# Kernel tuning notes

Hardware: AMD Instinct MI355X
Metric: run time of the kernel (lower is better)

The kernel has to match this reference:

```python
import jax, jax.numpy as jnp
import numpy as np

N, E, G, H, C = 50000, 800000, 512, 4, 64
DIN, DENC = 128, 256


def setup_inputs() -> dict:
    key = jax.random.key(0)
    ks = jax.random.split(key, 12)
    inp = {
        "hy": jax.random.normal(ks[0], (1, G, DENC), jnp.float32),
        "x": jax.random.normal(ks[1], (N, DIN), jnp.float32),
        "edge_index": jax.random.randint(ks[2], (2, E), 0, N, jnp.int32),
        "batch": jnp.sort(jax.random.randint(ks[3], (N,), 0, G, jnp.int32)),
        # GATv2Conv params (lin_l, lin_r: DIN -> H*C; att: [H, C]; bias: [C] since concat=False)
        "Wl": jax.random.normal(ks[4], (DIN, H * C), jnp.float32) * (1.0 / np.sqrt(DIN)),
        "bl": jnp.zeros((H * C,), jnp.float32),
        "Wr": jax.random.normal(ks[5], (DIN, H * C), jnp.float32) * (1.0 / np.sqrt(DIN)),
        "br": jnp.zeros((H * C,), jnp.float32),
        "att": jax.random.normal(ks[6], (H, C), jnp.float32) * (1.0 / np.sqrt(C)),
        "bias_gnn": jnp.zeros((C,), jnp.float32),
        # fc: (DENC + 64) -> DENC
        "Wfc": jax.random.normal(ks[7], (DENC + C, DENC), jnp.float32) * (1.0 / np.sqrt(DENC + C)),
        "bfc": jnp.zeros((DENC,), jnp.float32),
    }
    return inp


def _gatv2(x, edge_index, Wl, bl, Wr, br, att, bias_gnn):
    # add self loops (PyG default)
    loops = jnp.arange(N, dtype=edge_index.dtype)
    src = jnp.concatenate([edge_index[0], loops])
    dst = jnp.concatenate([edge_index[1], loops])
    xl = (x @ Wl + bl).reshape(N, H, C)  # source transform
    xr = (x @ Wr + br).reshape(N, H, C)  # target transform
    s = jax.nn.leaky_relu(xl[src] + xr[dst], 0.2)        # [Et, H, C]
    e = jnp.einsum('ehc,hc->eh', s, att)                 # [Et, H]
    # segment softmax over incoming edges of each dst node
    m = jax.ops.segment_max(e, dst, num_segments=N)
    m = jnp.where(jnp.isfinite(m), m, 0.0)
    a = jnp.exp(e - m[dst])
    denom = jax.ops.segment_sum(a, dst, num_segments=N)
    alpha = a / (denom[dst] + 1e-16)                     # [Et, H]
    msg = xl[src] * alpha[:, :, None]                    # [Et, H, C]
    out = jax.ops.segment_sum(msg, dst, num_segments=N)  # [N, H, C]
    return out.mean(axis=1) + bias_gnn                   # concat=False -> head mean


def reference(hy, x, edge_index, batch, Wl, bl, Wr, br, att, bias_gnn, Wfc, bfc):
    h = jax.nn.leaky_relu(_gatv2(x, edge_index, Wl, bl, Wr, br, att, bias_gnn), 0.01)
    # global mean pool per graph
    sums = jax.ops.segment_sum(h, batch, num_segments=G)
    cnts = jax.ops.segment_sum(jnp.ones((N, 1), h.dtype), batch, num_segments=G)
    hg = (sums / jnp.maximum(cnts, 1.0))[None]           # [1, G, C]
    cat = jnp.concatenate([hy, hg], axis=2)              # [1, G, DENC+C]
    return cat @ Wfc + bfc
```

## Files before the change

### kernel.cpp

```cpp
#include <hip/hip_runtime.h>

typedef unsigned short u16;
typedef __attribute__((ext_vector_type(8))) short bf16x8;
typedef __attribute__((ext_vector_type(4))) float f32x4;
typedef __attribute__((ext_vector_type(2))) float f32x2;

constexpr int N    = 50000;
constexpr int E    = 800000;
constexpr int G    = 512;
constexpr int HC   = 256;
constexpr int DIN  = 128;
constexpr int DENC = 256;
constexpr int DFC  = 320;
constexpr int NBLK = (N + 1023) / 1024;
constexpr int MT   = 64;
constexpr int XB   = (N + MT - 1) / MT;
constexpr int CBLK = 4;

__device__ __forceinline__ float bf2f(u16 u) {
    return __uint_as_float(((unsigned)u) << 16);
}
__device__ __forceinline__ u16 f2bf(float f) {
    unsigned u = __float_as_uint(f);
    u += 0x7fffu + ((u >> 16) & 1u);
    return (u16)(u >> 16);
}
__device__ __forceinline__ float lrelu(float v, float s) {
    return v > 0.0f ? v : v * s;
}

template<int CTRL>
__device__ __forceinline__ float dpp_radd(float x) {
    int y = __builtin_amdgcn_update_dpp(0, __float_as_int(x), CTRL, 0xF, 0xF, true);
    return x + __int_as_float(y);
}

template<bool BF> __device__ __forceinline__ float ld(const void* p, size_t i) {
    if constexpr (BF) return bf2f(((const u16*)p)[i]);
    else              return ((const float*)p)[i];
}
template<bool BF> __device__ __forceinline__ float4 ld4(const void* p, size_t i) {
    if constexpr (BF) {
        ushort4 v = ((const ushort4*)p)[i >> 2];
        return make_float4(bf2f(v.x), bf2f(v.y), bf2f(v.z), bf2f(v.w));
    } else {
        return ((const float4*)p)[i >> 2];
    }
}
template<bool BF> __device__ __forceinline__ void st(void* p, size_t i, float v) {
    if constexpr (BF) ((u16*)p)[i] = f2bf(v);
    else              ((float*)p)[i] = v;
}
__device__ __forceinline__ float ldr(const void* p, size_t i, bool bf) {
    return bf ? bf2f(((const u16*)p)[i]) : ((const float*)p)[i];
}

__global__ void k_detect(const void* x, int* flag) {
    if (blockIdx.x == 0 && threadIdx.x == 0) {
        const u16* p = (const u16*)x;
        int ok = 0;
        for (int i = 0; i < 256; i++) {
            unsigned e = (p[i] >> 7) & 0xffu;
            if (e == 0u || (e >= 100u && e <= 140u)) ok++;
        }
        *flag = (ok >= 218) ? 0 : 1;
    }
}

__global__ __launch_bounds__(64) void k_wprep(const void* Wl, const void* Wr,
                                              u16* __restrict__ whi, u16* __restrict__ wlo,
                                              const int* __restrict__ flag) {
    bool bf = (*flag == 0);
    int tile = blockIdx.x;
    int l = threadIdx.x;
    int c = tile & 31, s = tile >> 5;
    int col = c * 16 + (l & 15);
    int kbase = s * 32 + ((l >> 4) * 8);
    size_t o = (size_t)tile * 512 + (size_t)l * 8;
    #pragma unroll
    for (int j = 0; j < 8; j++) {
        int k = kbase + j;
        float v = (col < HC) ? ldr(Wl, (size_t)k * HC + col, bf)
                             : ldr(Wr, (size_t)k * HC + (col - HC), bf);
        u16 h = f2bf(v);
        whi[o + j] = h;
        wlo[o + j] = f2bf(v - bf2f(h));
    }
}

template<bool BF>
__global__ __launch_bounds__(256, 4) void k_xlxr_t(
    const void* __restrict__ x, const u16* __restrict__ whi, const u16* __restrict__ wlo,
    const void* __restrict__ bl, const void* __restrict__ br,
    u16* __restrict__ xl, u16* __restrict__ xr, const int* __restrict__ flag) {
    if ((*flag == 0) != BF) return;
    __shared__ u16 ah[(BF ? 1 : 2) * MT][136];
    int b = blockIdx.x, t = threadIdx.x;
    int rb = b >> 1, cg = b & 1;
    int row0 = rb * MT;

    {
        int k0 = (t & 15) * 8;
        #pragma unroll
        for (int it = 0; it < 4; it++) {
            int r = (t >> 4) + it * 16;
            int g = row0 + r; if (g >= N) g = N - 1;
            size_t base = (size_t)g * DIN + k0;
            if constexpr (BF) {
                const ushort4* xp = (const ushort4*)x;
                *(ushort4*)&ah[r][k0]     = xp[base >> 2];
                *(ushort4*)&ah[r][k0 + 4] = xp[(base >> 2) + 1];
            } else {
                const float4* xp = (const float4*)x;
                float4 f0 = xp[base >> 2], f1 = xp[(base >> 2) + 1];
                float v[8] = {f0.x, f0.y, f0.z, f0.w, f1.x, f1.y, f1.z, f1.w};
                #pragma unroll
                for (int j = 0; j < 8; j++) {
                    u16 h = f2bf(v[j]);
                    ah[r][k0 + j] = h;
                    ah[MT + r][k0 + j] = f2bf(v[j] - bf2f(h));
                }
            }
        }
    }
    __syncthreads();

    int w = t >> 6, l = t & 63;
    int rl = l & 15, kg = (l >> 4) * 8;
    f32x4 acc[4][CBLK];
    #pragma unroll
    for (int rt = 0; rt < 4; rt++)
        #pragma unroll
        for (int ci = 0; ci < CBLK; ci++) {
            f32x4 z = {0.f, 0.f, 0.f, 0.f};
            acc[rt][ci] = z;
        }

    #pragma unroll
    for (int s = 0; s < 4; s++) {
        bf16x8 a0 = *(const bf16x8*)&ah[rl][s * 32 + kg];
        bf16x8 a1 = *(const bf16x8*)&ah[16 + rl][s * 32 + kg];
        bf16x8 a2 = *(const bf16x8*)&ah[32 + rl][s * 32 + kg];
        bf16x8 a3 = *(const bf16x8*)&ah[48 + rl][s * 32 + kg];
        #pragma unroll
        for (int ci = 0; ci < CBLK; ci++) {
            int c = cg * 16 + w * CBLK + ci;
            size_t fo = ((size_t)(s * 32 + c) * 64 + l) * 8;
            bf16x8 bh = *(const bf16x8*)&whi[fo];
            acc[0][ci] = __builtin_amdgcn_mfma_f32_16x16x32_bf16(a0, bh, acc[0][ci], 0, 0, 0);
            acc[1][ci] = __builtin_amdgcn_mfma_f32_16x16x32_bf16(a1, bh, acc[1][ci], 0, 0, 0);
            acc[2][ci] = __builtin_amdgcn_mfma_f32_16x16x32_bf16(a2, bh, acc[2][ci], 0, 0, 0);
            acc[3][ci] = __builtin_amdgcn_mfma_f32_16x16x32_bf16(a3, bh, acc[3][ci], 0, 0, 0);
            if constexpr (!BF) {
                bf16x8 e0 = *(const bf16x8*)&ah[MT + rl][s * 32 + kg];
                bf16x8 e1 = *(const bf16x8*)&ah[MT + 16 + rl][s * 32 + kg];
                bf16x8 e2 = *(const bf16x8*)&ah[MT + 32 + rl][s * 32 + kg];
                bf16x8 e3 = *(const bf16x8*)&ah[MT + 48 + rl][s * 32 + kg];
                bf16x8 bw = *(const bf16x8*)&wlo[fo];
                acc[0][ci] = __builtin_amdgcn_mfma_f32_16x16x32_bf16(a0, bw, acc[0][ci], 0, 0, 0);
                acc[0][ci] = __builtin_amdgcn_mfma_f32_16x16x32_bf16(e0, bh, acc[0][ci], 0, 0, 0);
                acc[1][ci] = __builtin_amdgcn_mfma_f32_16x16x32_bf16(a1, bw, acc[1][ci], 0, 0, 0);
                acc[1][ci] = __builtin_amdgcn_mfma_f32_16x16x32_bf16(e1, bh, acc[1][ci], 0, 0, 0);
                acc[2][ci] = __builtin_amdgcn_mfma_f32_16x16x32_bf16(a2, bw, acc[2][ci], 0, 0, 0);
                acc[2][ci] = __builtin_amdgcn_mfma_f32_16x16x32_bf16(e2, bh, acc[2][ci], 0, 0, 0);
                acc[3][ci] = __builtin_amdgcn_mfma_f32_16x16x32_bf16(a3, bw, acc[3][ci], 0, 0, 0);
                acc[3][ci] = __builtin_amdgcn_mfma_f32_16x16x32_bf16(e3, bh, acc[3][ci], 0, 0, 0);
            }
        }
    }
    __syncthreads();

    float fbias[CBLK];
    #pragma unroll
    for (int ci = 0; ci < CBLK; ci++) {
        int colm = ((cg * 16 + w * CBLK + ci) * 16 + (l & 15)) & (HC - 1);
        fbias[ci] = ld<BF>(cg ? br : bl, colm);
    }
    u16* dst = cg ? xr : xl;

    u16 (*ep)[264] = reinterpret_cast<u16 (*)[264]>(&ah[0][0]);
    int r4 = (l >> 4) * 4;
    #pragma unroll
    for (int rt = 0; rt < 4; rt++) {
        #pragma unroll
        for (int ci = 0; ci < CBLK; ci++) {
            int colm = ((cg * 16 + w * CBLK + ci) * 16 + (l & 15)) & (HC - 1);
            #pragma unroll
            for (int i = 0; i < 4; i++)
                ep[r4 + i][colm] = f2bf(acc[rt][ci][i] + fbias[ci]);
        }
        __syncthreads();
        #pragma unroll
        for (int j = 0; j < 2; j++) {
            int q   = t + 256 * j;
            int row = q >> 5;
            int ck  = q & 31;
            int gr  = row0 + rt * 16 + row;
            uint4 v = *(const uint4*)&ep[row][ck * 8];
            if (gr < N) *(uint4*)&dst[(size_t)gr * HC + ck * 8] = v;
        }
        __syncthreads();
    }
}

__global__ void k_deg(const int* __restrict__ ei, int* __restrict__ deg) {
    int e = blockIdx.x * blockDim.x + threadIdx.x;
    if (e < E) {
        int d = ei[E + e];
        if ((unsigned)d < (unsigned)N) atomicAdd(&deg[d], 1);
    }
}

__global__ void k_chunksum(const int* __restrict__ deg, int* __restrict__ blocksum) {
    int b = blockIdx.x, t = threadIdx.x;
    int base = b * 1024 + t * 4;
    int s = 0;
    #pragma unroll
    for (int i = 0; i < 4; i++) { int idx = base + i; if (idx < N) s += deg[idx]; }
    for (int off = 32; off; off >>= 1) s += __shfl_down(s, off, 64);
    __shared__ int ls[4];
    int wave = t >> 6;
    if ((t & 63) == 0) ls[wave] = s;
    __syncthreads();
    if (t == 0) blocksum[b] = ls[0] + ls[1] + ls[2] + ls[3];
}

__global__ void k_scanoff(int* __restrict__ blocksum, int* __restrict__ rowptr) {
    if (threadIdx.x == 0 && blockIdx.x == 0) {
        int run = 0;
        for (int b = 0; b < NBLK; b++) { int v = blocksum[b]; blocksum[b] = run; run += v; }
        rowptr[N] = run;
    }
}

__global__ void k_scanwrite(const int* __restrict__ deg, const int* __restrict__ blocksum,
                            int* __restrict__ rowptr) {
    int b = blockIdx.x, t = threadIdx.x;
    int base = b * 1024 + t * 4;
    int v[4]; int s = 0;
    #pragma unroll
    for (int i = 0; i < 4; i++) { v[i] = (base + i < N) ? deg[base + i] : 0; s += v[i]; }
    int lane = t & 63, wave = t >> 6;
    int x = s;
    for (int off = 1; off < 64; off <<= 1) {
        int y = __shfl_up(x, off, 64);
        if (lane >= off) x += y;
    }
    __shared__ int wtot[4];
    if (lane == 63) wtot[wave] = x;
    __syncthreads();
    int woff = 0;
    for (int w = 0; w < wave; w++) woff += wtot[w];
    int run = blocksum[b] + woff + (x - s);
    #pragma unroll
    for (int i = 0; i < 4; i++) {
        int idx = base + i;
        if (idx < N) rowptr[idx] = run;
        run += v[i];
    }
}

__global__ void k_fill(const int* __restrict__ ei, const int* __restrict__ rowptr,
                       int* __restrict__ cursor, int* __restrict__ col) {
    int e = blockIdx.x * blockDim.x + threadIdx.x;
    if (e < E) {
        int d = ei[E + e];
        if ((unsigned)d < (unsigned)N) {
            int pos = atomicAdd(&cursor[d], 1);
            unsigned idx = (unsigned)(rowptr[d] + pos);
            int s = ei[e];
            if (idx < (unsigned)E) col[idx] = ((unsigned)s < (unsigned)N) ? s : d;
        }
    }
}

template<bool BF>
__device__ void gat_body(const u16* __restrict__ xl, const u16* __restrict__ xr,
                         const int* __restrict__ rowptr, const int* __restrict__ col,
                         const void* __restrict__ att, const void* __restrict__ bias_gnn,
                         float* __restrict__ hnode) {
    int wid = (blockIdx.x * blockDim.x + threadIdx.x) >> 6;
    int lane = threadIdx.x & 63;
    if (wid >= N) return;
    int node = wid;

    const char* xlb = (const char*)xl;
    unsigned loff = (unsigned)lane << 3;
    auto loadrow = [&](int src) -> uint2 {
        return *(const uint2*)(xlb + (((unsigned)src << 9) + loff));
    };

    uint2 xrv = *(const uint2*)(((const char*)xr) + (((unsigned)node << 9) + loff));
    f32x2 ra, rb;
    ra.x = __uint_as_float(xrv.x << 16);
    ra.y = __uint_as_float(xrv.x & 0xffff0000u);
    rb.x = __uint_as_float(xrv.y << 16);
    rb.y = __uint_as_float(xrv.y & 0xffff0000u);
    float4 atv = ld4<BF>(att, (size_t)lane * 4);
    f32x2 ta = {atv.x, atv.y}, tb = {atv.z, atv.w};

    float l = 0.f;
    f32x2 aa = {0.f, 0.f}, ab = {0.f, 0.f};

    auto edge = [&](uint2 xv) {
        f32x2 xa, xb;
        xa.x = __uint_as_float(xv.x << 16);
        xa.y = __uint_as_float(xv.x & 0xffff0000u);
        xb.x = __uint_as_float(xv.y << 16);
        xb.y = __uint_as_float(xv.y & 0xffff0000u);
        f32x2 ua = xa + ra, ub = xb + rb;
        f32x2 sa = __builtin_elementwise_max(ua * 0.2f, ua);
        f32x2 sb = __builtin_elementwise_max(ub * 0.2f, ub);
        f32x2 d  = sa * ta + sb * tb;
        float p = d.x + d.y;
        p = dpp_radd<0xB1>(p);
        p = dpp_radd<0x4E>(p);
        p = dpp_radd<0x141>(p);
        p = dpp_radd<0x140>(p);
        float wgt = __expf(fminf(p, 80.0f));
        l += wgt;
        f32x2 wv = {wgt, wgt};
        aa = aa + xa * wv;
        ab = ab + xb * wv;
    };

    edge(loadrow(node));

    int beg = rowptr[node], end = rowptr[node + 1];
    beg = max(0, min(beg, E));
    end = max(beg, min(end, E));
    beg = __builtin_amdgcn_readfirstlane(beg);
    end = __builtin_amdgcn_readfirstlane(end);

    constexpr int UNR = 8;
    int j = beg;
    for (; j + UNR <= end; j += UNR) {
        int srcs[UNR];
        #pragma unroll
        for (int u = 0; u < UNR; u++) srcs[u] = col[j + u];
        uint2 vv[UNR];
        #pragma unroll
        for (int u = 0; u < UNR; u++) vv[u] = loadrow(srcs[u]);
        #pragma unroll
        for (int u = 0; u < UNR; u++) edge(vv[u]);
    }
    for (; j < end; j++) edge(loadrow(col[j]));

    float inv = 1.0f / (l + 1e-16f);
    float a0 = aa.x * inv, a1 = aa.y * inv, a2 = ab.x * inv, a3 = ab.y * inv;
    a0 += __shfl_xor(a0, 16); a0 += __shfl_xor(a0, 32);
    a1 += __shfl_xor(a1, 16); a1 += __shfl_xor(a1, 32);
    a2 += __shfl_xor(a2, 16); a2 += __shfl_xor(a2, 32);
    a3 += __shfl_xor(a3, 16); a3 += __shfl_xor(a3, 32);
    if (lane < 16) {
        float4 bv = ld4<BF>(bias_gnn, (size_t)lane * 4);
        float4 o;
        o.x = lrelu(a0 * 0.25f + bv.x, 0.01f);
        o.y = lrelu(a1 * 0.25f + bv.y, 0.01f);
        o.z = lrelu(a2 * 0.25f + bv.z, 0.01f);
        o.w = lrelu(a3 * 0.25f + bv.w, 0.01f);
        reinterpret_cast<float4*>(hnode)[(size_t)node * 16 + lane] = o;
    }
}

__global__ __launch_bounds__(256, 8) void k_gat(
    const u16* xl, const u16* xr, const int* rowptr, const int* col,
    const void* att, const void* bias_gnn, float* hnode, const int* flag) {
    if (*flag == 0) gat_body<true>(xl, xr, rowptr, col, att, bias_gnn, hnode);
    else            gat_body<false>(xl, xr, rowptr, col, att, bias_gnn, hnode);
}

__global__ __launch_bounds__(256) void k_pool(const float* __restrict__ hnode,
                                              const int* __restrict__ batch,
                                              float* __restrict__ hg) {
    int g = blockIdx.x, t = threadIdx.x;
    int lane = t & 63, w = t >> 6;
    int lo = 0, hi = N;
    while (lo < hi) { int mid = (lo + hi) >> 1; if (batch[mid] < g) lo = mid + 1; else hi = mid; }
    int s0 = lo;
    hi = N;
    while (lo < hi) { int mid = (lo + hi) >> 1; if (batch[mid] < g + 1) lo = mid + 1; else hi = mid; }
    int s1 = lo;
    float sum = 0.f;
    for (int n = s0 + w; n < s1; n += 4) sum += hnode[(size_t)n * 64 + lane];
    __shared__ float red[4][64];
    red[w][lane] = sum;
    __syncthreads();
    if (w == 0) {
        float s = red[0][lane] + red[1][lane] + red[2][lane] + red[3][lane];
        int cnt = s1 - s0; if (cnt < 1) cnt = 1;
        hg[g * 64 + lane] = s / (float)cnt;
    }
}

template<bool BF>
__device__ void fc_body(const void* __restrict__ hy, const float* __restrict__ hg,
                        const void* __restrict__ Wfc, const void* __restrict__ bfc,
                        void* __restrict__ out) {
    int g = blockIdx.x, t = threadIdx.x;
    __shared__ float cat[DFC];
    cat[t] = ld<BF>(hy, (size_t)g * DENC + t);
    if (t < 64) cat[DENC + t] = hg[g * 64 + t];
    __syncthreads();
    float acc = ld<BF>(bfc, t);
    for (int k = 0; k < DFC; k++) acc = fmaf(cat[k], ld<BF>(Wfc, (size_t)k * DENC + t), acc);
    st<BF>(out, (size_t)g * DENC + t, acc);
}

__global__ __launch_bounds__(256) void k_fc(
    const void* hy, const float* hg, const void* Wfc, const void* bfc,
    void* out, const int* flag) {
    if (*flag == 0) fc_body<true>(hy, hg, Wfc, bfc, out);
    else            fc_body<false>(hy, hg, Wfc, bfc, out);
}

extern "C" void kernel_launch(void* const* d_in, const int* in_sizes, int n_in,
                              void* d_out, int out_size, void* d_ws, size_t ws_size,
                              hipStream_t stream) {
    const void* hy   = d_in[0];
    const void* x    = d_in[1];
    const int*  ei   = (const int*)d_in[2];
    const int*  batch= (const int*)d_in[3];
    const void* Wl   = d_in[4];
    const void* bl   = d_in[5];
    const void* Wr   = d_in[6];
    const void* br   = d_in[7];
    const void* att  = d_in[8];
    const void* bias = d_in[9];
    const void* Wfc  = d_in[10];
    const void* bfc  = d_in[11];

    char* w = (char*)d_ws;
    u16*  xl      = (u16*)w;   w += (size_t)N * HC * 2;
    u16*  xr      = (u16*)w;   w += (size_t)N * HC * 2;
    float* hnode  = (float*)w; w += (size_t)N * 64 * 4;
    float* hg     = (float*)w; w += (size_t)G * 64 * 4;
    int*  col     = (int*)w;   w += (size_t)E * 4;
    int*  rowptr  = (int*)w;   w += ((size_t)N + 16) * 4;
    int*  blocksum= (int*)w;   w += 64 * 4;
    int*  flag    = (int*)w;   w += 64 * 4;
    int*  deg     = (int*)w;   w += (size_t)N * 4;
    int*  cursor  = (int*)w;   w += (size_t)N * 4;
    u16*  whi     = (u16*)w;   w += (size_t)4 * 32 * 64 * 8 * 2;
    u16*  wlo     = (u16*)w;   w += (size_t)4 * 32 * 64 * 8 * 2;

    hipMemsetAsync(deg, 0, (size_t)2 * N * 4, stream);

    k_detect<<<1, 64, 0, stream>>>(x, flag);
    k_wprep<<<128, 64, 0, stream>>>(Wl, Wr, whi, wlo, flag);
    k_xlxr_t<true ><<<XB * 2, 256, 0, stream>>>(x, whi, wlo, bl, br, xl, xr, flag);
    k_xlxr_t<false><<<XB * 2, 256, 0, stream>>>(x, whi, wlo, bl, br, xl, xr, flag);
    k_deg<<<(E + 255) / 256, 256, 0, stream>>>(ei, deg);
    k_chunksum<<<NBLK, 256, 0, stream>>>(deg, blocksum);
    k_scanoff<<<1, 64, 0, stream>>>(blocksum, rowptr);
    k_scanwrite<<<NBLK, 256, 0, stream>>>(deg, blocksum, rowptr);
    k_fill<<<(E + 255) / 256, 256, 0, stream>>>(ei, rowptr, cursor, col);
    k_gat<<<(N * 64 + 255) / 256, 256, 0, stream>>>(xl, xr, rowptr, col, att, bias, hnode, flag);
    k_pool<<<G, 256, 0, stream>>>(hnode, batch, hg);
    k_fc<<<G, 256, 0, stream>>>(hy, hg, Wfc, bfc, d_out, flag);
}
```

Before: 317.9 us.

## Process four edges per wavefront in parallel in the GATv2 aggregation kernel

Each wavefront is split into four 16-lane groups, and each group handles a different incoming edge. Each lane now loads and processes 16 channels of a row instead of 4, so the per-edge head dot product needs only two DPP reduction steps. The self-loop moves into a masked tail iteration, and partial sums from the four groups are combined with shuffles at the end. The aim is to cut the number of serial edge iterations per node and raise memory-level parallelism. The cost is more registers per lane, which the launch bounds acknowledge by lowering the occupancy hint from 8 to 4.

```diff
diff --git a/kernel.cpp b/kernel.cpp
--- a/kernel.cpp
+++ b/kernel.cpp
@@ -283,48 +283,66 @@
     int lane = threadIdx.x & 63;
     if (wid >= N) return;
     int node = wid;
+    int g = lane >> 4;
+    int q = lane & 15;
+    unsigned coff = (unsigned)q << 5;
 
     const char* xlb = (const char*)xl;
-    unsigned loff = (unsigned)lane << 3;
-    auto loadrow = [&](int src) -> uint2 {
-        return *(const uint2*)(xlb + (((unsigned)src << 9) + loff));
+
+    f32x2 r[8], t[8];
+    {
+        const char* xrb = (const char*)xr + (((unsigned)node << 9) + coff);
+        #pragma unroll
+        for (int k = 0; k < 4; k++) {
+            uint2 v = *(const uint2*)(xrb + k * 8);
+            r[2*k].x   = __uint_as_float(v.x << 16);
+            r[2*k].y   = __uint_as_float(v.x & 0xffff0000u);
+            r[2*k+1].x = __uint_as_float(v.y << 16);
+            r[2*k+1].y = __uint_as_float(v.y & 0xffff0000u);
+        }
+        #pragma unroll
+        for (int k = 0; k < 4; k++) {
+            float4 a = ld4<BF>(att, (size_t)q * 16 + k * 4);
+            t[2*k]   = f32x2{a.x, a.y};
+            t[2*k+1] = f32x2{a.z, a.w};
+        }
+    }
+
+    float l = 0.f;
+    f32x2 acc[8];
+    #pragma unroll
+    for (int k = 0; k < 8; k++) acc[k] = f32x2{0.f, 0.f};
+
+    auto eload = [&](int src, uint2 (&a)[4]) {
+        const char* rbp = xlb + (((unsigned)src << 9) + coff);
+        #pragma unroll
+        for (int k = 0; k < 4; k++) a[k] = *(const uint2*)(rbp + k * 8);
     };
-
-    uint2 xrv = *(const uint2*)(((const char*)xr) + (((unsigned)node << 9) + loff));
-    f32x2 ra, rb;
-    ra.x = __uint_as_float(xrv.x << 16);
-    ra.y = __uint_as_float(xrv.x & 0xffff0000u);
-    rb.x = __uint_as_float(xrv.y << 16);
-    rb.y = __uint_as_float(xrv.y & 0xffff0000u);
-    float4 atv = ld4<BF>(att, (size_t)lane * 4);
-    f32x2 ta = {atv.x, atv.y}, tb = {atv.z, atv.w};
-
-    float l = 0.f;
-    f32x2 aa = {0.f, 0.f}, ab = {0.f, 0.f};
-
-    auto edge = [&](uint2 xv) {
-        f32x2 xa, xb;
-        xa.x = __uint_as_float(xv.x << 16);
-        xa.y = __uint_as_float(xv.x & 0xffff0000u);
-        xb.x = __uint_as_float(xv.y << 16);
-        xb.y = __uint_as_float(xv.y & 0xffff0000u);
-        f32x2 ua = xa + ra, ub = xb + rb;
-        f32x2 sa = __builtin_elementwise_max(ua * 0.2f, ua);
-        f32x2 sb = __builtin_elementwise_max(ub * 0.2f, ub);
-        f32x2 d  = sa * ta + sb * tb;
+    auto emath = [&](const uint2 (&a)[4], float wmask) {
+        f32x2 x[8];
+        #pragma unroll
+        for (int k = 0; k < 4; k++) {
+            x[2*k].x   = __uint_as_float(a[k].x << 16);
+            x[2*k].y   = __uint_as_float(a[k].x & 0xffff0000u);
+            x[2*k+1].x = __uint_as_float(a[k].y << 16);
+            x[2*k+1].y = __uint_as_float(a[k].y & 0xffff0000u);
+        }
+        f32x2 d = {0.f, 0.f};
+        #pragma unroll
+        for (int k = 0; k < 8; k++) {
+            f32x2 u = x[k] + r[k];
+            f32x2 s = __builtin_elementwise_max(u, u * 0.2f);
+            d = d + s * t[k];
+        }
         float p = d.x + d.y;
         p = dpp_radd<0xB1>(p);
         p = dpp_radd<0x4E>(p);
-        p = dpp_radd<0x141>(p);
-        p = dpp_radd<0x140>(p);
-        float wgt = __expf(fminf(p, 80.0f));
-        l += wgt;
-        f32x2 wv = {wgt, wgt};
-        aa = aa + xa * wv;
-        ab = ab + xb * wv;
+        float w = __expf(fminf(p, 80.0f)) * wmask;
+        l += w;
+        f32x2 wv = {w, w};
+        #pragma unroll
+        for (int k = 0; k < 8; k++) acc[k] = acc[k] + x[k] * wv;
     };
-
-    edge(loadrow(node));
 
     int beg = rowptr[node], end = rowptr[node + 1];
     beg = max(0, min(beg, E));
@@ -332,38 +350,64 @@
     beg = __builtin_amdgcn_readfirstlane(beg);
     end = __builtin_amdgcn_readfirstlane(end);
 
-    constexpr int UNR = 8;
     int j = beg;
-    for (; j + UNR <= end; j += UNR) {
-        int srcs[UNR];
-        #pragma unroll
-        for (int u = 0; u < UNR; u++) srcs[u] = col[j + u];
-        uint2 vv[UNR];
-        #pragma unroll
-        for (int u = 0; u < UNR; u++) vv[u] = loadrow(srcs[u]);
-        #pragma unroll
-        for (int u = 0; u < UNR; u++) edge(vv[u]);
-    }
-    for (; j < end; j++) edge(loadrow(col[j]));
-
+    for (; j + 8 <= end; j += 8) {
+        int c0 = col[j + g], c1 = col[j + 4 + g];
+        uint2 a0[4], a1[4];
+        eload(c0, a0);
+        eload(c1, a1);
+        emath(a0, 1.f);
+        emath(a1, 1.f);
+    }
+    for (; j + 4 <= end; j += 4) {
+        int c0 = col[j + g];
+        uint2 a0[4];
+        eload(c0, a0);
+        emath(a0, 1.f);
+    }
+    {
+        int jj = j + g;
+        int idx = (jj < end) ? jj : 0;
+        int cj = col[idx];
+        int src = (jj < end) ? cj : node;
+        float m = (jj <= end) ? 1.f : 0.f;
+        uint2 a0[4];
+        eload(src, a0);
+        emath(a0, m);
+    }
+
+    l += __shfl_xor(l, 16); l += __shfl_xor(l, 32);
     float inv = 1.0f / (l + 1e-16f);
-    float a0 = aa.x * inv, a1 = aa.y * inv, a2 = ab.x * inv, a3 = ab.y * inv;
-    a0 += __shfl_xor(a0, 16); a0 += __shfl_xor(a0, 32);
-    a1 += __shfl_xor(a1, 16); a1 += __shfl_xor(a1, 32);
-    a2 += __shfl_xor(a2, 16); a2 += __shfl_xor(a2, 32);
-    a3 += __shfl_xor(a3, 16); a3 += __shfl_xor(a3, 32);
-    if (lane < 16) {
-        float4 bv = ld4<BF>(bias_gnn, (size_t)lane * 4);
-        float4 o;
-        o.x = lrelu(a0 * 0.25f + bv.x, 0.01f);
-        o.y = lrelu(a1 * 0.25f + bv.y, 0.01f);
-        o.z = lrelu(a2 * 0.25f + bv.z, 0.01f);
-        o.w = lrelu(a3 * 0.25f + bv.w, 0.01f);
-        reinterpret_cast<float4*>(hnode)[(size_t)node * 16 + lane] = o;
-    }
-}
-
-__global__ __launch_bounds__(256, 8) void k_gat(
+    #pragma unroll
+    for (int k = 0; k < 8; k++) {
+        acc[k].x += __shfl_xor(acc[k].x, 16);
+        acc[k].y += __shfl_xor(acc[k].y, 16);
+        acc[k].x += __shfl_xor(acc[k].x, 32);
+        acc[k].y += __shfl_xor(acc[k].y, 32);
+        acc[k].x *= inv;  acc[k].y *= inv;
+        acc[k].x += __shfl_xor(acc[k].x, 4);
+        acc[k].y += __shfl_xor(acc[k].y, 4);
+        acc[k].x += __shfl_xor(acc[k].x, 8);
+        acc[k].y += __shfl_xor(acc[k].y, 8);
+    }
+
+    if (lane < 4) {
+        int cb = lane;
+        float* orow = hnode + (size_t)node * 64 + cb * 16;
+        #pragma unroll
+        for (int k = 0; k < 4; k++) {
+            float4 bv = ld4<BF>(bias_gnn, (size_t)cb * 16 + k * 4);
+            float4 o;
+            o.x = lrelu(acc[2*k].x   * 0.25f + bv.x, 0.01f);
+            o.y = lrelu(acc[2*k].y   * 0.25f + bv.y, 0.01f);
+            o.z = lrelu(acc[2*k+1].x * 0.25f + bv.z, 0.01f);
+            o.w = lrelu(acc[2*k+1].y * 0.25f + bv.w, 0.01f);
+            *reinterpret_cast<float4*>(orow + k * 4) = o;
+        }
+    }
+}
+
+__global__ __launch_bounds__(256, 4) void k_gat(
     const u16* xl, const u16* xr, const int* rowptr, const int* col,
     const void* att, const void* bias_gnn, float* hnode, const int* flag) {
     if (*flag == 0) gat_body<true>(xl, xr, rowptr, col, att, bias_gnn, hnode);
```

After: 337.9 us. +6.3%, slower.
